# Kernel optimization log

Measured on AMD Instinct MI355X. Metric: run time of the kernel, lower is better.

The kernel has to match this reference:

```python
import jax, jax.numpy as jnp
import numpy as np

B, C, H, W = 2, 192, 256, 256
HEADS = 6


def _conv1x1(x, w, b):
    # x: [b,ci,h,w], w: [co,ci,1,1], b: [co]
    return jnp.einsum('oi,bihw->bohw', w[:, :, 0, 0], x) + b[None, :, None, None]


def _dwconv3x3(x, w, b):
    # depthwise 3x3, padding=1; x: [b,c,h,w], w: [c,1,3,3], b: [c]
    y = jax.lax.conv_general_dilated(
        x, w, window_strides=(1, 1), padding='SAME',
        feature_group_count=x.shape[1],
        dimension_numbers=('NCHW', 'OIHW', 'NCHW'))
    return y + b[None, :, None, None]


def _l2norm(t, eps=1e-12):
    # F.normalize(dim=-1): x / max(||x||_2, eps)
    n = jnp.sqrt(jnp.sum(t * t, axis=-1, keepdims=True))
    return t / jnp.maximum(n, eps)


def setup_inputs() -> dict:
    key = jax.random.key(0)
    ks = jax.random.split(key, 12)
    s = 0.02
    return {
        'feat_guide': jax.random.normal(ks[0], (B, C, H, W), jnp.float32),
        'feat_op': jax.random.normal(ks[1], (B, C, H, W), jnp.float32),
        'q_w': jax.random.normal(ks[2], (C, C, 1, 1), jnp.float32) * s,
        'q_b': jax.random.normal(ks[3], (C,), jnp.float32) * s,
        'kv_w': jax.random.normal(ks[4], (2 * C, C, 1, 1), jnp.float32) * s,
        'kv_b': jax.random.normal(ks[5], (2 * C,), jnp.float32) * s,
        'q_dw_w': jax.random.normal(ks[6], (C, 1, 3, 3), jnp.float32) * s,
        'q_dw_b': jax.random.normal(ks[7], (C,), jnp.float32) * s,
        'kv_dw_w': jax.random.normal(ks[8], (2 * C, 1, 3, 3), jnp.float32) * s,
        'kv_dw_b': jax.random.normal(ks[9], (2 * C,), jnp.float32) * s,
        'proj_w': jax.random.normal(ks[10], (C, C, 1, 1), jnp.float32) * s,
        'proj_b': jax.random.normal(ks[11], (C,), jnp.float32) * s,
        'temperature': jnp.ones((HEADS, 1, 1), jnp.float32),
    }


def reference(feat_guide, feat_op, q_w, q_b, kv_w, kv_b, q_dw_w, q_dw_b,
              kv_dw_w, kv_dw_b, proj_w, proj_b, temperature):
    b, c, h, w = feat_guide.shape
    q = _dwconv3x3(_conv1x1(feat_guide, q_w, q_b), q_dw_w, q_dw_b)
    kv = _dwconv3x3(_conv1x1(feat_op, kv_w, kv_b), kv_dw_w, kv_dw_b)
    k, v = jnp.split(kv, 2, axis=1)

    def heads(t):  # [b,c,h,w] -> [b,heads,c/heads,hw]
        return t.reshape(b, HEADS, c // HEADS, h * w)

    q = _l2norm(heads(q))
    k = _l2norm(heads(k))
    v = heads(v)
    # channel-wise attention: [b,heads,c',c'] scores over hw
    attn = jnp.einsum('bhcn,bhdn->bhcd', q, k) * temperature[None]
    attn = jax.nn.softmax(attn, axis=-1)
    out = jnp.einsum('bhcd,bhdn->bhcn', attn, v).reshape(b, c, h, w)
    return _conv1x1(out, proj_w, proj_b)
```

## Files before the change

### kernel.cpp

```cpp
#include <hip/hip_runtime.h>

#define HW_N 65536
#define CC 192
#define NCHUNKS 256

typedef __attribute__((ext_vector_type(8))) short short8v;
typedef __attribute__((ext_vector_type(4))) short short4v;
typedef __attribute__((ext_vector_type(4))) float f32x4;
typedef __attribute__((ext_vector_type(4))) int int4v;

__device__ __forceinline__ float bf2f(unsigned short u) {
  union { unsigned int i; float f; } v; v.i = ((unsigned int)u) << 16; return v.f;
}
__device__ __forceinline__ unsigned short f2bf(float f) {
  union { float f; unsigned int i; } v; v.f = f;
  unsigned int r = v.i + 0x7fffu + ((v.i >> 16) & 1u);
  return (unsigned short)(r >> 16);
}

__global__ __launch_bounds__(256) void cvt_w(
    const float* __restrict__ qw, const float* __restrict__ kvw,
    unsigned short* __restrict__ Wq, unsigned short* __restrict__ Wkv) {
  const int i = (blockIdx.x * 256 + threadIdx.x) * 8;
  const float* src; unsigned short* dst; int off;
  if (i < 36864) { src = qw; dst = Wq; off = i; }
  else { src = kvw; dst = Wkv; off = i - 36864; }
  unsigned short tmp[8];
#pragma unroll
  for (int j = 0; j < 8; ++j) tmp[j] = f2bf(src[off + j]);
  *(short8v*)(dst + off) = *(short8v*)tmp;
}

template <int INF32, int OUTF32, int PERB>
__global__ __launch_bounds__(512) void conv_gemm(
    const void* __restrict__ X_, const unsigned short* __restrict__ W,
    const float* __restrict__ bias, void* __restrict__ out_,
    int Mtot, int msplit) {
  __shared__ __align__(16) unsigned char smem[51200];
  typedef unsigned short row200[200];
  typedef unsigned short row152[152];
  row200* Bt = (row200*)smem;
  row152* Rp = (row152*)smem;
  const int d = blockIdx.x;
  int mt, nt;
  if (msplit == 2) { mt = (d >> 3) & 1; nt = (d & 7) | ((d >> 4) << 3); }
  else { mt = 0; nt = d; }
  const int m0 = mt * 192, n0 = nt * 128;
  const int b = blockIdx.z;
  const int t = threadIdx.x;
  const int lane = t & 63, wv = t >> 6;
  const int l15 = lane & 15, lg = lane >> 4;
  const int wm = wv & 3, wn = wv >> 2;
  const int mrow = m0 + wm * 48;
  const int nw = wn * 64;
  const size_t xbase = (size_t)b * CC * (size_t)HW_N + n0;
  const unsigned short* Wb = W + (PERB ? (size_t)b * Mtot * CC : 0);

  for (int task = t; task < 768; task += 512) {
    const int kp = task >> 5, nq = task & 31;
    unsigned int p[8][2];
    if (INF32) {
      const float* Xf = (const float*)X_;
#pragma unroll
      for (int j = 0; j < 8; ++j) {
        f32x4 v = *(const f32x4*)(Xf + xbase + (size_t)(kp * 8 + j) * HW_N + nq * 4);
        p[j][0] = (unsigned int)f2bf(v[0]) | ((unsigned int)f2bf(v[1]) << 16);
        p[j][1] = (unsigned int)f2bf(v[2]) | ((unsigned int)f2bf(v[3]) << 16);
      }
    } else {
      const unsigned short* Xh = (const unsigned short*)X_;
#pragma unroll
      for (int j = 0; j < 8; ++j) {
        short4v v = *(const short4v*)(Xh + xbase + (size_t)(kp * 8 + j) * HW_N + nq * 4);
        p[j][0] = (unsigned int)(unsigned short)v[0] | ((unsigned int)(unsigned short)v[1] << 16);
        p[j][1] = (unsigned int)(unsigned short)v[2] | ((unsigned int)(unsigned short)v[3] << 16);
      }
    }
    const int kpx = kp ^ (nq & 7);
#pragma unroll
    for (int nn = 0; nn < 4; ++nn) {
      unsigned int q4[4];
#pragma unroll
      for (int wi = 0; wi < 4; ++wi) {
        const unsigned int lo = (p[2 * wi][nn >> 1] >> ((nn & 1) * 16)) & 0xffffu;
        const unsigned int hi = (p[2 * wi + 1][nn >> 1] >> ((nn & 1) * 16)) & 0xffffu;
        q4[wi] = lo | (hi << 16);
      }
      *(int4v*)&Bt[nq * 4 + nn][kpx * 8] = *(int4v*)q4;
    }
  }
  __syncthreads();

  f32x4 acc[3][4] = {};
#pragma unroll
  for (int kc = 0; kc < 6; ++kc) {
    const int k0 = kc * 32 + lg * 8;
    short8v af[3], bfr[4];
#pragma unroll
    for (int fr = 0; fr < 3; ++fr)
      af[fr] = *(const short8v*)(Wb + (size_t)(mrow + fr * 16 + l15) * CC + k0);
#pragma unroll
    for (int fc = 0; fc < 4; ++fc) {
      const int row = nw + fc * 16 + l15;
      const int oct = (kc * 4 + lg) ^ ((row >> 2) & 7);
      bfr[fc] = *(const short8v*)&Bt[row][oct * 8];
    }
#pragma unroll
    for (int fr = 0; fr < 3; ++fr)
#pragma unroll
      for (int fc = 0; fc < 4; ++fc)
        acc[fr][fc] = __builtin_amdgcn_mfma_f32_16x16x32_bf16(af[fr], bfr[fc], acc[fr][fc], 0, 0, 0);
  }

  const size_t obase = (size_t)b * Mtot * (size_t)HW_N;
  if (OUTF32) {
    float* outf = (float*)out_;
#pragma unroll
    for (int fr = 0; fr < 3; ++fr) {
      const int rbase = mrow + fr * 16 + lg * 4;
#pragma unroll
      for (int r = 0; r < 4; ++r) {
        const float bb = bias[rbase + r];
        const size_t ro = obase + (size_t)(rbase + r) * HW_N + n0 + nw;
#pragma unroll
        for (int fc = 0; fc < 4; ++fc)
          outf[ro + fc * 16 + l15] = acc[fr][fc][r] + bb;
      }
    }
    return;
  }
  __syncthreads();

#pragma unroll
  for (int half = 0; half < 2; ++half) {
    if ((wm >> 1) == half) {
      const int mbase = (wm & 1) * 48;
#pragma unroll
      for (int fr = 0; fr < 3; ++fr) {
#pragma unroll
        for (int r = 0; r < 4; ++r) {
          const int mloc = mbase + fr * 16 + lg * 4 + r;
          const float bb = bias[m0 + half * 96 + mloc];
#pragma unroll
          for (int fc = 0; fc < 4; ++fc)
            Rp[mloc][nw + fc * 16 + l15] = f2bf(acc[fr][fc][r] + bb);
        }
      }
    }
    __syncthreads();
#pragma unroll
    for (int s = 0; s < 3; ++s) {
      const int idx = s * 512 + t;
      const int m = idx >> 4, n8 = (idx & 15) * 8;
      short8v v = *(short8v*)&Rp[m][n8];
      const size_t oo = obase + (size_t)(m0 + half * 96 + m) * HW_N + n0 + n8;
      *(short8v*)((unsigned short*)out_ + oo) = v;
    }
    __syncthreads();
  }
}

__global__ __launch_bounds__(256) void dwconv3x3_all(
    const unsigned short* __restrict__ QC, const unsigned short* __restrict__ KVC,
    const float* __restrict__ q_dw_w, const float* __restrict__ q_dw_b,
    const float* __restrict__ kv_dw_w, const float* __restrict__ kv_dw_b,
    unsigned short* __restrict__ Qb, unsigned short* __restrict__ Kb,
    unsigned short* __restrict__ Vb) {
  const int t = threadIdx.x;
  const int wc = (t & 31) * 8;
  const int h0 = blockIdx.x * 16 + (t >> 5) * 2;
  const int y = blockIdx.y, b = blockIdx.z;
  const unsigned short* in; const float* w; float bv; unsigned short* out;
  if (y < 192) {
    in = QC + ((size_t)b * 192 + y) * (size_t)HW_N;
    w = q_dw_w + y * 9; bv = q_dw_b[y];
    out = Qb + ((size_t)b * 192 + y) * (size_t)HW_N;
  } else if (y < 384) {
    const int c = y - 192;
    in = KVC + ((size_t)b * 384 + c) * (size_t)HW_N;
    w = kv_dw_w + c * 9; bv = kv_dw_b[c];
    out = Kb + ((size_t)b * 192 + c) * (size_t)HW_N;
  } else {
    const int c = y - 384;
    in = KVC + ((size_t)b * 384 + 192 + c) * (size_t)HW_N;
    w = kv_dw_w + (192 + c) * 9; bv = kv_dw_b[192 + c];
    out = Vb + ((size_t)b * 192 + c) * (size_t)HW_N;
  }
  float wv9[9];
#pragma unroll
  for (int i = 0; i < 9; ++i) wv9[i] = w[i];
  float f[4][10];
#pragma unroll
  for (int ky = 0; ky < 4; ++ky) {
    const int hh = h0 + ky - 1;
    if (hh < 0 || hh > 255) {
#pragma unroll
      for (int j = 0; j < 10; ++j) f[ky][j] = 0.f;
    } else {
      const unsigned short* row = in + hh * 256;
      short8v v = *(const short8v*)(row + wc);
      f[ky][0] = (wc > 0) ? bf2f(row[wc - 1]) : 0.f;
#pragma unroll
      for (int j = 0; j < 8; ++j) f[ky][1 + j] = bf2f((unsigned short)v[j]);
      f[ky][9] = (wc < 248) ? bf2f(row[wc + 8]) : 0.f;
    }
  }
#pragma unroll
  for (int rr = 0; rr < 2; ++rr) {
    union { short8v v; unsigned short u[8]; } o;
#pragma unroll
    for (int j = 0; j < 8; ++j) {
      float acc = bv;
#pragma unroll
      for (int ky = 0; ky < 3; ++ky)
#pragma unroll
        for (int kx = 0; kx < 3; ++kx)
          acc += wv9[ky * 3 + kx] * f[rr + ky][j + kx];
      o.u[j] = f2bf(acc);
    }
    *(short8v*)(out + (h0 + rr) * 256 + wc) = o.v;
  }
}

__global__ __launch_bounds__(64) void gram_kernel(
    const unsigned short* __restrict__ Q, const unsigned short* __restrict__ K,
    float* __restrict__ Gp, float* __restrict__ nqp, float* __restrict__ nkp) {
  const int lane = threadIdx.x;
  const int l15 = lane & 15, lg = lane >> 4;
  const int chunk = blockIdx.x, h = blockIdx.y, b = blockIdx.z;
  const int bh = b * 6 + h;
  const size_t base = ((size_t)b * CC + h * 32) * (size_t)HW_N;
  f32x4 acc[2][2] = {};
  float sq[2] = {0.f, 0.f}, sk[2] = {0.f, 0.f};
  const int nst = chunk * 256 + lg * 8;
  for (int ks = 0; ks < 8; ++ks) {
    const int n = nst + ks * 32;
    short8v qa[2], kb[2];
#pragma unroll
    for (int fr = 0; fr < 2; ++fr) {
      qa[fr] = *(const short8v*)(Q + base + (size_t)(fr * 16 + l15) * HW_N + n);
      kb[fr] = *(const short8v*)(K + base + (size_t)(fr * 16 + l15) * HW_N + n);
    }
#pragma unroll
    for (int fr = 0; fr < 2; ++fr)
#pragma unroll
      for (int j = 0; j < 8; ++j) {
        float a = bf2f((unsigned short)qa[fr][j]); sq[fr] += a * a;
        float c2 = bf2f((unsigned short)kb[fr][j]); sk[fr] += c2 * c2;
      }
#pragma unroll
    for (int fr = 0; fr < 2; ++fr)
#pragma unroll
      for (int fc = 0; fc < 2; ++fc)
        acc[fr][fc] = __builtin_amdgcn_mfma_f32_16x16x32_bf16(qa[fr], kb[fc], acc[fr][fc], 0, 0, 0);
  }
  float* Gb = Gp + (size_t)(chunk * 12 + bh) * 1024;
#pragma unroll
  for (int fr = 0; fr < 2; ++fr)
#pragma unroll
    for (int fc = 0; fc < 2; ++fc)
#pragma unroll
      for (int r = 0; r < 4; ++r)
        Gb[(fr * 16 + lg * 4 + r) * 32 + fc * 16 + l15] = acc[fr][fc][r];
#pragma unroll
  for (int fr = 0; fr < 2; ++fr) {
    float v = sq[fr]; v += __shfl_down(v, 32); v += __shfl_down(v, 16);
    float u = sk[fr]; u += __shfl_down(u, 32); u += __shfl_down(u, 16);
    if (lane < 16) {
      nqp[(size_t)(chunk * 12 + bh) * 32 + fr * 16 + lane] = v;
      nkp[(size_t)(chunk * 12 + bh) * 32 + fr * 16 + lane] = u;
    }
  }
}

__global__ __launch_bounds__(256) void reduce_gram(
    const float* __restrict__ Gp, const float* __restrict__ nqp, const float* __restrict__ nkp,
    float* __restrict__ G, float* __restrict__ nq, float* __restrict__ nk) {
  const int i = blockIdx.x * 256 + threadIdx.x;
  if (i < 12 * 1024) {
    float s = 0.f;
    for (int ch = 0; ch < NCHUNKS; ++ch) s += Gp[(size_t)ch * 12288 + i];
    G[i] = s;
  } else if (i < 12 * 1024 + 384) {
    const int j = i - 12 * 1024;
    float s = 0.f;
    for (int ch = 0; ch < NCHUNKS; ++ch) s += nqp[(size_t)ch * 384 + j];
    nq[j] = s;
  } else if (i < 12 * 1024 + 768) {
    const int j = i - 12 * 1024 - 384;
    float s = 0.f;
    for (int ch = 0; ch < NCHUNKS; ++ch) s += nkp[(size_t)ch * 384 + j];
    nk[j] = s;
  }
}

__global__ __launch_bounds__(256) void attn_proj(
    const float* __restrict__ G, const float* __restrict__ nq, const float* __restrict__ nk,
    const float* __restrict__ temp, const float* __restrict__ proj_w,
    unsigned short* __restrict__ Mout) {
  const int h = blockIdx.x, b = blockIdx.y;
  const int bh = b * 6 + h;
  const int t = threadIdx.x;
  __shared__ float sc[32][33];
  __shared__ float nrmq[32], nrmk[32];
  if (t < 32) nrmq[t] = fmaxf(sqrtf(nq[bh * 32 + t]), 1e-12f);
  else if (t < 64) nrmk[t - 32] = fmaxf(sqrtf(nk[bh * 32 + t - 32]), 1e-12f);
  __syncthreads();
  const float tpr = temp[h];
  for (int i = t; i < 1024; i += 256) {
    const int c = i >> 5, d = i & 31;
    sc[c][d] = G[bh * 1024 + i] * tpr / (nrmq[c] * nrmk[d]);
  }
  __syncthreads();
  if (t < 32) {
    float mx = -1e30f;
    for (int d = 0; d < 32; ++d) mx = fmaxf(mx, sc[t][d]);
    float sum = 0.f;
    for (int d = 0; d < 32; ++d) { float e = __expf(sc[t][d] - mx); sc[t][d] = e; sum += e; }
    const float inv = 1.f / sum;
    for (int d = 0; d < 32; ++d) sc[t][d] *= inv;
  }
  __syncthreads();
  for (int i = t; i < 6144; i += 256) {
    const int co = i >> 5, d = i & 31;
    float acc = 0.f;
    for (int c = 0; c < 32; ++c) acc += proj_w[co * CC + h * 32 + c] * sc[c][d];
    Mout[((size_t)b * CC + co) * CC + h * 32 + d] = f2bf(acc);
  }
}

extern "C" void kernel_launch(void* const* d_in, const int* in_sizes, int n_in,
                              void* d_out, int out_size, void* d_ws, size_t ws_size,
                              hipStream_t stream) {
  const float* fg = (const float*)d_in[0];
  const float* fo = (const float*)d_in[1];
  const float* q_w = (const float*)d_in[2];
  const float* q_b = (const float*)d_in[3];
  const float* kv_w = (const float*)d_in[4];
  const float* kv_b = (const float*)d_in[5];
  const float* q_dw_w = (const float*)d_in[6];
  const float* q_dw_b = (const float*)d_in[7];
  const float* kv_dw_w = (const float*)d_in[8];
  const float* kv_dw_b = (const float*)d_in[9];
  const float* proj_w = (const float*)d_in[10];
  const float* proj_b = (const float*)d_in[11];
  const float* temp = (const float*)d_in[12];

  char* ws = (char*)d_ws;
  unsigned short* QC  = (unsigned short*)(ws + 0);
  unsigned short* KVC = (unsigned short*)(ws + 50331648);
  unsigned short* Qb  = (unsigned short*)(ws + 150994944);
  unsigned short* Kb  = (unsigned short*)(ws + 0);
  unsigned short* Vb  = (unsigned short*)(ws + 50331648);
  float* Gp  = (float*)(ws + 100663296);
  float* nqp = (float*)(ws + 113246208);
  float* nkp = (float*)(ws + 113639424);
  float* G   = (float*)(ws + 208011264);
  float* nqv = (float*)(ws + 208060416);
  float* nkv = (float*)(ws + 208061952);
  unsigned short* Mw  = (unsigned short*)(ws + 208063488);
  unsigned short* Wq  = (unsigned short*)(ws + 208210944);
  unsigned short* Wkv = (unsigned short*)(ws + 208284672);

  cvt_w<<<dim3(54), dim3(256), 0, stream>>>(q_w, kv_w, Wq, Wkv);
  conv_gemm<1, 0, 0><<<dim3(512, 1, 2), dim3(512), 0, stream>>>(
      (const void*)fg, Wq, q_b, (void*)QC, 192, 1);
  conv_gemm<1, 0, 0><<<dim3(1024, 1, 2), dim3(512), 0, stream>>>(
      (const void*)fo, Wkv, kv_b, (void*)KVC, 384, 2);
  dwconv3x3_all<<<dim3(16, 576, 2), dim3(256), 0, stream>>>(
      QC, KVC, q_dw_w, q_dw_b, kv_dw_w, kv_dw_b, Qb, Kb, Vb);
  gram_kernel<<<dim3(NCHUNKS, 6, 2), dim3(64), 0, stream>>>(Qb, Kb, Gp, nqp, nkp);
  reduce_gram<<<dim3(51), dim3(256), 0, stream>>>(Gp, nqp, nkp, G, nqv, nkv);
  attn_proj<<<dim3(6, 2), dim3(256), 0, stream>>>(G, nqv, nkv, temp, proj_w, Mw);
  conv_gemm<0, 1, 1><<<dim3(512, 1, 2), dim3(512), 0, stream>>>(
      (const void*)Vb, Mw, proj_b, d_out, 192, 1);
}
```

Measured before the change: 273.2 us.

## Fuse Q/K depthwise conv into Gram kernel, keep separate V dwconv

The 3x3 depthwise conv for Q and K is now computed on the fly inside the Gram-matrix kernel, one image row per block, so the intermediate Q and K bf16 tensors are never written to or re-read from global memory. Only V still goes through a standalone dwconv kernel, and the workspace layout is adjusted to match. This removes a large round-trip of HBM traffic. In exchange, each Gram block re-reads three input rows per fragment (halo reads served mostly by cache) and does more ALU work per lane, with more register pressure.

```diff
diff --git a/kernel.cpp b/kernel.cpp
--- a/kernel.cpp
+++ b/kernel.cpp
@@ -160,32 +160,17 @@
   }
 }
 
-__global__ __launch_bounds__(256) void dwconv3x3_all(
-    const unsigned short* __restrict__ QC, const unsigned short* __restrict__ KVC,
-    const float* __restrict__ q_dw_w, const float* __restrict__ q_dw_b,
-    const float* __restrict__ kv_dw_w, const float* __restrict__ kv_dw_b,
-    unsigned short* __restrict__ Qb, unsigned short* __restrict__ Kb,
-    unsigned short* __restrict__ Vb) {
+__global__ __launch_bounds__(256) void dwconv3x3_v(
+    const unsigned short* __restrict__ KVC, const float* __restrict__ kv_dw_w,
+    const float* __restrict__ kv_dw_b, unsigned short* __restrict__ Vb) {
   const int t = threadIdx.x;
   const int wc = (t & 31) * 8;
   const int h0 = blockIdx.x * 16 + (t >> 5) * 2;
-  const int y = blockIdx.y, b = blockIdx.z;
-  const unsigned short* in; const float* w; float bv; unsigned short* out;
-  if (y < 192) {
-    in = QC + ((size_t)b * 192 + y) * (size_t)HW_N;
-    w = q_dw_w + y * 9; bv = q_dw_b[y];
-    out = Qb + ((size_t)b * 192 + y) * (size_t)HW_N;
-  } else if (y < 384) {
-    const int c = y - 192;
-    in = KVC + ((size_t)b * 384 + c) * (size_t)HW_N;
-    w = kv_dw_w + c * 9; bv = kv_dw_b[c];
-    out = Kb + ((size_t)b * 192 + c) * (size_t)HW_N;
-  } else {
-    const int c = y - 384;
-    in = KVC + ((size_t)b * 384 + 192 + c) * (size_t)HW_N;
-    w = kv_dw_w + (192 + c) * 9; bv = kv_dw_b[192 + c];
-    out = Vb + ((size_t)b * 192 + c) * (size_t)HW_N;
-  }
+  const int c = blockIdx.y, b = blockIdx.z;
+  const unsigned short* in = KVC + ((size_t)b * 384 + 192 + c) * (size_t)HW_N;
+  const float* w = kv_dw_w + (192 + c) * 9;
+  const float bv = kv_dw_b[192 + c];
+  unsigned short* out = Vb + ((size_t)b * CC + c) * (size_t)HW_N;
   float wv9[9];
 #pragma unroll
   for (int i = 0; i < 9; ++i) wv9[i] = w[i];
@@ -222,53 +207,104 @@
   }
 }
 
-__global__ __launch_bounds__(64) void gram_kernel(
-    const unsigned short* __restrict__ Q, const unsigned short* __restrict__ K,
+__device__ __forceinline__ short8v dwfrag(
+    const unsigned short* __restrict__ chan, int r, int w0,
+    const float* wv, float bv, float& ssq) {
+  float fv[3][10];
+#pragma unroll
+  for (int ky = 0; ky < 3; ++ky) {
+    const int rr = r + ky - 1;
+    if (rr < 0 || rr > 255) {
+#pragma unroll
+      for (int j = 0; j < 10; ++j) fv[ky][j] = 0.f;
+    } else {
+      const unsigned short* rp = chan + rr * 256;
+      short8v v = *(const short8v*)(rp + w0);
+      fv[ky][0] = (w0 > 0) ? bf2f(rp[w0 - 1]) : 0.f;
+#pragma unroll
+      for (int j = 0; j < 8; ++j) fv[ky][1 + j] = bf2f((unsigned short)v[j]);
+      fv[ky][9] = (w0 < 248) ? bf2f(rp[w0 + 8]) : 0.f;
+    }
+  }
+  union { short8v v; unsigned short u[8]; } o;
+#pragma unroll
+  for (int j = 0; j < 8; ++j) {
+    float a = bv;
+#pragma unroll
+    for (int ky = 0; ky < 3; ++ky)
+#pragma unroll
+      for (int kx = 0; kx < 3; ++kx)
+        a += wv[ky * 3 + kx] * fv[ky][j + kx];
+    const unsigned short us = f2bf(a);
+    o.u[j] = us;
+    const float q = bf2f(us);
+    ssq += q * q;
+  }
+  return o.v;
+}
+
+__global__ __launch_bounds__(64) void gram_fused(
+    const unsigned short* __restrict__ QC, const unsigned short* __restrict__ KVC,
+    const float* __restrict__ q_dw_w, const float* __restrict__ q_dw_b,
+    const float* __restrict__ kv_dw_w, const float* __restrict__ kv_dw_b,
     float* __restrict__ Gp, float* __restrict__ nqp, float* __restrict__ nkp) {
   const int lane = threadIdx.x;
   const int l15 = lane & 15, lg = lane >> 4;
-  const int chunk = blockIdx.x, h = blockIdx.y, b = blockIdx.z;
+  const int r = blockIdx.x, h = blockIdx.y, b = blockIdx.z;
   const int bh = b * 6 + h;
-  const size_t base = ((size_t)b * CC + h * 32) * (size_t)HW_N;
+  int cc2[2];
+  cc2[0] = h * 32 + l15; cc2[1] = h * 32 + 16 + l15;
+  float wq[2][9], wk[2][9], bq[2], bk[2];
+#pragma unroll
+  for (int fr = 0; fr < 2; ++fr) {
+#pragma unroll
+    for (int i = 0; i < 9; ++i) {
+      wq[fr][i] = q_dw_w[cc2[fr] * 9 + i];
+      wk[fr][i] = kv_dw_w[cc2[fr] * 9 + i];
+    }
+    bq[fr] = q_dw_b[cc2[fr]];
+    bk[fr] = kv_dw_b[cc2[fr]];
+  }
+  const unsigned short* qch[2];
+  const unsigned short* kch[2];
+#pragma unroll
+  for (int fr = 0; fr < 2; ++fr) {
+    qch[fr] = QC + ((size_t)b * CC + cc2[fr]) * (size_t)HW_N;
+    kch[fr] = KVC + ((size_t)b * 384 + cc2[fr]) * (size_t)HW_N;
+  }
+
   f32x4 acc[2][2] = {};
   float sq[2] = {0.f, 0.f}, sk[2] = {0.f, 0.f};
-  const int nst = chunk * 256 + lg * 8;
+#pragma unroll
   for (int ks = 0; ks < 8; ++ks) {
-    const int n = nst + ks * 32;
+    const int w0 = lg * 8 + ks * 32;
     short8v qa[2], kb[2];
 #pragma unroll
     for (int fr = 0; fr < 2; ++fr) {
-      qa[fr] = *(const short8v*)(Q + base + (size_t)(fr * 16 + l15) * HW_N + n);
-      kb[fr] = *(const short8v*)(K + base + (size_t)(fr * 16 + l15) * HW_N + n);
-    }
-#pragma unroll
-    for (int fr = 0; fr < 2; ++fr)
-#pragma unroll
-      for (int j = 0; j < 8; ++j) {
-        float a = bf2f((unsigned short)qa[fr][j]); sq[fr] += a * a;
-        float c2 = bf2f((unsigned short)kb[fr][j]); sk[fr] += c2 * c2;
-      }
+      qa[fr] = dwfrag(qch[fr], r, w0, wq[fr], bq[fr], sq[fr]);
+      kb[fr] = dwfrag(kch[fr], r, w0, wk[fr], bk[fr], sk[fr]);
+    }
 #pragma unroll
     for (int fr = 0; fr < 2; ++fr)
 #pragma unroll
       for (int fc = 0; fc < 2; ++fc)
         acc[fr][fc] = __builtin_amdgcn_mfma_f32_16x16x32_bf16(qa[fr], kb[fc], acc[fr][fc], 0, 0, 0);
   }
-  float* Gb = Gp + (size_t)(chunk * 12 + bh) * 1024;
+  float* Gb = Gp + (size_t)(r * 12 + bh) * 1024;
 #pragma unroll
   for (int fr = 0; fr < 2; ++fr)
 #pragma unroll
     for (int fc = 0; fc < 2; ++fc)
 #pragma unroll
-      for (int r = 0; r < 4; ++r)
-        Gb[(fr * 16 + lg * 4 + r) * 32 + fc * 16 + l15] = acc[fr][fc][r];
+      for (int rr = 0; rr < 4; ++rr)
+        Gb[(fr * 16 + lg * 4 + rr) * 32 + fc * 16 + l15] = acc[fr][fc][rr];
 #pragma unroll
   for (int fr = 0; fr < 2; ++fr) {
     float v = sq[fr]; v += __shfl_down(v, 32); v += __shfl_down(v, 16);
     float u = sk[fr]; u += __shfl_down(u, 32); u += __shfl_down(u, 16);
     if (lane < 16) {
-      nqp[(size_t)(chunk * 12 + bh) * 32 + fr * 16 + lane] = v;
-      nkp[(size_t)(chunk * 12 + bh) * 32 + fr * 16 + lane] = u;
+      nqp[(size_t)(r * 12 + bh) * 32 + fr * 16 + lane] = v;
+      nkp[(size_t)(r * 12 + bh) * 32 + fr * 16 + lane] = u;
     }
   }
 }
@@ -349,12 +385,10 @@
   char* ws = (char*)d_ws;
   unsigned short* QC  = (unsigned short*)(ws + 0);
   unsigned short* KVC = (unsigned short*)(ws + 50331648);
-  unsigned short* Qb  = (unsigned short*)(ws + 150994944);
-  unsigned short* Kb  = (unsigned short*)(ws + 0);
-  unsigned short* Vb  = (unsigned short*)(ws + 50331648);
-  float* Gp  = (float*)(ws + 100663296);
-  float* nqp = (float*)(ws + 113246208);
-  float* nkp = (float*)(ws + 113639424);
+  unsigned short* Vb  = (unsigned short*)(ws + 0);
+  float* Gp  = (float*)(ws + 150994944);
+  float* nqp = (float*)(ws + 163577856);
+  float* nkp = (float*)(ws + 163971072);
   float* G   = (float*)(ws + 208011264);
   float* nqv = (float*)(ws + 208060416);
   float* nkv = (float*)(ws + 208061952);
@@ -367,9 +401,10 @@
       (const void*)fg, Wq, q_b, (void*)QC, 192, 1);
   conv_gemm<1, 0, 0><<<dim3(1024, 1, 2), dim3(512), 0, stream>>>(
       (const void*)fo, Wkv, kv_b, (void*)KVC, 384, 2);
-  dwconv3x3_all<<<dim3(16, 576, 2), dim3(256), 0, stream>>>(
-      QC, KVC, q_dw_w, q_dw_b, kv_dw_w, kv_dw_b, Qb, Kb, Vb);
-  gram_kernel<<<dim3(NCHUNKS, 6, 2), dim3(64), 0, stream>>>(Qb, Kb, Gp, nqp, nkp);
+  gram_fused<<<dim3(256, 6, 2), dim3(64), 0, stream>>>(
+      QC, KVC, q_dw_w, q_dw_b, kv_dw_w, kv_dw_b, Gp, nqp, nkp);
+  dwconv3x3_v<<<dim3(16, 192, 2), dim3(256), 0, stream>>>(
+      KVC, kv_dw_w, kv_dw_b, Vb);
   reduce_gram<<<dim3(51), dim3(256), 0, stream>>>(Gp, nqp, nkp, G, nqv, nkv);
   attn_proj<<<dim3(6, 2), dim3(256), 0, stream>>>(G, nqv, nkv, temp, proj_w, Mw);
   conv_gemm<0, 1, 1><<<dim3(512, 1, 2), dim3(512), 0, stream>>>(
```

After: 390.4 us. 42.9% more time.
